# Optimization experiments

Hardware: AMD Instinct MI355X
Metric: run time of the kernel (lower is better)

Reference implementation:

```python
import jax, jax.numpy as jnp
import numpy as np

B, S, D = 2, 2048, 1024
H = 16
DK = D // H
SCALE = 1.0 / np.sqrt(DK)

def setup_inputs() -> dict:
    key = jax.random.key(0)
    ks = jax.random.split(key, 11)
    std = 1.0 / np.sqrt(D)
    return {
        "query": jax.random.normal(ks[0], (B, S, D), jnp.float32),
        "key":   jax.random.normal(ks[1], (B, S, D), jnp.float32),
        "value": jax.random.normal(ks[2], (B, S, D), jnp.float32),
        "Wq": jax.random.normal(ks[3], (D, H * DK), jnp.float32) * std,
        "bq": jnp.zeros((H * DK,), jnp.float32),
        "Wk": jax.random.normal(ks[4], (D, H * DK), jnp.float32) * std,
        "bk": jnp.zeros((H * DK,), jnp.float32),
        "Wv": jax.random.normal(ks[5], (D, H * DK), jnp.float32) * std,
        "bv": jnp.zeros((H * DK,), jnp.float32),
        "Wo": jax.random.normal(ks[6], (D, D), jnp.float32) * std,
        "bo": jnp.zeros((D,), jnp.float32),
    }

def reference(query, key, value, Wq, bq, Wk, bk, Wv, bv, Wo, bo):
    b, s, _ = query.shape
    # projections -> [b, s, h, d_k]
    q = (query @ Wq + bq).reshape(b, s, H, DK)
    k = (key   @ Wk + bk).reshape(b, s, H, DK)
    v = (value @ Wv + bv).reshape(b, s, H, DK)
    # scores [b, i, j, h]
    scores = jnp.einsum('bihd,bjhd->bijh', q, k) * SCALE
    attn = jax.nn.softmax(scores, axis=2)  # softmax over key dim j
    # dropout rate 0.0 (eval mode) -> identity
    x = jnp.einsum('bijh,bjhd->bihd', attn, v).reshape(b, s, H * DK)
    return x @ Wo + bo
```

## Files before the change

kernel.cpp:

```cpp
#include <hip/hip_runtime.h>
#include <hip/hip_bf16.h>
#include <math.h>
#include <stdint.h>

constexpr int Bb = 2, Ss = 2048, Dd = 1024, Hh = 16;
constexpr int Mm = Bb * Ss;
constexpr int Nn = Dd;
constexpr int Kk = Dd;
constexpr float QSCALE = 0.125f * 1.44269504088896340736f;

typedef unsigned short ushort_t;
typedef __attribute__((ext_vector_type(8))) short bf16x8;
typedef __attribute__((ext_vector_type(4))) float f32x4;

#if __has_builtin(__builtin_amdgcn_exp2f)
#define EXP2F(x) __builtin_amdgcn_exp2f(x)
#else
#define EXP2F(x) exp2f(x)
#endif

__device__ __forceinline__ ushort_t f2bf(float f) {
  union { float f; unsigned u; } v; v.f = f;
  return (ushort_t)((v.u + 0x7fff + ((v.u >> 16) & 1)) >> 16);
}

__device__ __forceinline__ void load16_lds(const void* g, void* l) {
  __builtin_amdgcn_global_load_lds(
      (const __attribute__((address_space(1))) void*)(uintptr_t)g,
      (__attribute__((address_space(3))) void*)(uint32_t)(uintptr_t)l, 16, 0, 0);
}

__global__ __launch_bounds__(256) void prep(
    const float* __restrict__ q, const float* __restrict__ k,
    const float* __restrict__ v, ushort_t* __restrict__ qkvb,
    const float* __restrict__ Wq, const float* __restrict__ Wk,
    const float* __restrict__ Wv, const float* __restrict__ Wo,
    ushort_t* __restrict__ Wt) {
  const int bid = blockIdx.x;
  const int tid = threadIdx.x;
  if (bid < 12288) {
    const int z = bid >> 12, xi = bid & 4095;
    const float* src = (z == 0) ? q : (z == 1) ? k : v;
    ushort_t* dst = qkvb + (size_t)z * Mm * Kk;
    const size_t idx = ((size_t)xi * 256 + tid) * 4;
    const float4 val = *(const float4*)(src + idx);
    ushort4 o;
    o.x = f2bf(val.x); o.y = f2bf(val.y); o.z = f2bf(val.z); o.w = f2bf(val.w);
    *(ushort4*)(dst + idx) = o;
    return;
  }
  const int bid2 = bid - 12288;
  const int z = bid2 >> 8, rem = bid2 & 255;
  const float* W = (z == 0) ? Wq : (z == 1) ? Wk : (z == 2) ? Wv : Wo;
  ushort_t* out = Wt + (size_t)z * Kk * Nn;
  __shared__ float t[64][65];
  const int n0 = (rem & 15) * 64, k0 = (rem >> 4) * 64;
  const int lr = tid >> 4, lc = (tid & 15) * 4;
#pragma unroll
  for (int i = 0; i < 4; i++) {
    const int r = lr + i * 16;
    const float4 vv = *(const float4*)(W + (size_t)(k0 + r) * Nn + n0 + lc);
    t[r][lc] = vv.x; t[r][lc + 1] = vv.y; t[r][lc + 2] = vv.z; t[r][lc + 3] = vv.w;
  }
  __syncthreads();
  const int n = tid >> 2, kc = (tid & 3) * 16;
  ushort_t tmp[16];
#pragma unroll
  for (int j = 0; j < 16; j++) tmp[j] = f2bf(t[kc + j][n]);
  ushort_t* op = out + (size_t)(n0 + n) * Kk + k0 + kc;
  ((uint4*)op)[0] = ((uint4*)tmp)[0];
  ((uint4*)op)[1] = ((uint4*)tmp)[1];
}

__global__ __launch_bounds__(256) void transpose_v(
    const ushort_t* __restrict__ Vp, ushort_t* __restrict__ Vt) {
  __shared__ ushort_t t[64][68];
  const int tid = threadIdx.x;
  const int s0 = blockIdx.x * 64, h = blockIdx.y, b = blockIdx.z;
  const int lr = tid >> 4, lc = (tid & 15) * 4;
#pragma unroll
  for (int i = 0; i < 4; i++) {
    const int r = lr + i * 16;
    const ushort4 v =
        *(const ushort4*)(Vp + (size_t)(b * Ss + s0 + r) * Dd + h * 64 + lc);
    *(ushort4*)&t[r][lc] = v;
  }
  __syncthreads();
  const int d = tid >> 2, sc = (tid & 3) * 16;
  ushort_t tmp[16];
#pragma unroll
  for (int j = 0; j < 16; j++) tmp[j] = t[sc + j][d];
  ushort_t* op = Vt + ((size_t)b * Dd + h * 64 + d) * Ss + s0 + sc;
  ((uint4*)op)[0] = ((uint4*)tmp)[0];
  ((uint4*)op)[1] = ((uint4*)tmp)[1];
}

template <int BN, bool OUT_BF16>
__global__ __launch_bounds__(256) void gemm_mfma(
    const ushort_t* __restrict__ Abase, size_t a_stride,
    const ushort_t* __restrict__ Wbase, size_t w_stride,
    const float* __restrict__ bias0, const float* __restrict__ bias1,
    const float* __restrict__ bias2, void* __restrict__ Cbase, size_t c_stride,
    float scale_z0) {
  constexpr int BM = 128, BK = 32;
  constexpr int WM = (BN == 128) ? 64 : 32;
  constexpr int MT_ = WM / 16, NT_ = 4;
  __shared__ ushort_t As[BM * BK];
  __shared__ ushort_t Bs[BN * BK];
  const int tid = threadIdx.x, lane = tid & 63, wid = tid >> 6;
  const int z = blockIdx.z;
  const ushort_t* A = Abase + (size_t)z * a_stride;
  const ushort_t* Wt = Wbase + (size_t)z * w_stride;
  const float* bias = (z == 0) ? bias0 : (z == 1) ? bias1 : bias2;
  const float sc = (z == 0) ? scale_z0 : 1.0f;
  const int m0 = blockIdx.y * BM, n0 = blockIdx.x * BN;
  const int wm = (BN == 128) ? (wid >> 1) * 64 : wid * 32;
  const int wn = (BN == 128) ? (wid & 1) * 64 : 0;
  const int quad = lane >> 4, r16 = lane & 15;
  const int srow = lane >> 2;
  const int scol = (lane & 3) * 8;

  f32x4 acc[MT_][NT_];
#pragma unroll
  for (int m = 0; m < MT_; m++)
#pragma unroll
    for (int n = 0; n < NT_; n++) acc[m][n] = f32x4{0.f, 0.f, 0.f, 0.f};

  for (int k0 = 0; k0 < Kk; k0 += BK) {
    __syncthreads();
#pragma unroll
    for (int i = 0; i < BM / 64; i++) {
      const int I = wid * (BM / 64) + i;
      load16_lds(A + (size_t)(m0 + I * 16 + srow) * Kk + k0 + scol, As + I * 512);
    }
#pragma unroll
    for (int i = 0; i < BN / 64; i++) {
      const int I = wid * (BN / 64) + i;
      load16_lds(Wt + (size_t)(n0 + I * 16 + srow) * Kk + k0 + scol, Bs + I * 512);
    }
    __syncthreads();
    bf16x8 af[MT_], bfr[NT_];
#pragma unroll
    for (int m = 0; m < MT_; m++)
      af[m] = *(const bf16x8*)(As + (wm + m * 16 + r16) * BK + quad * 8);
#pragma unroll
    for (int n = 0; n < NT_; n++)
      bfr[n] = *(const bf16x8*)(Bs + (wn + n * 16 + r16) * BK + quad * 8);
#pragma unroll
    for (int m = 0; m < MT_; m++)
#pragma unroll
      for (int n = 0; n < NT_; n++)
        acc[m][n] =
            __builtin_amdgcn_mfma_f32_16x16x32_bf16(af[m], bfr[n], acc[m][n], 0, 0, 0);
  }

#pragma unroll
  for (int m = 0; m < MT_; m++) {
#pragma unroll
    for (int n = 0; n < NT_; n++) {
      const int gc = n0 + wn + n * 16 + r16;
      const float bv = bias[gc];
#pragma unroll
      for (int r = 0; r < 4; r++) {
        const int gr = m0 + wm + m * 16 + quad * 4 + r;
        const float v = (acc[m][n][r] + bv) * sc;
        if (OUT_BF16)
          ((ushort_t*)Cbase)[(size_t)z * c_stride + (size_t)gr * Nn + gc] = f2bf(v);
        else
          ((float*)Cbase)[(size_t)z * c_stride + (size_t)gr * Nn + gc] = v;
      }
    }
  }
}

__global__ __launch_bounds__(256) void flash_mfma(
    const ushort_t* __restrict__ Qp, const ushort_t* __restrict__ Kp,
    const ushort_t* __restrict__ Vt, ushort_t* __restrict__ Xp) {
  __shared__ ushort_t Ks[64 * 64];
  __shared__ ushort_t Vts[64 * 64];
  __shared__ ushort_t Ps[64 * 72];
  const int tid = threadIdx.x, lane = tid & 63, wid = tid >> 6;
  const int qt = blockIdx.x, h = blockIdx.y, b = blockIdx.z;
  const int quad = lane >> 4, r16 = lane & 15;
  const int row8 = lane >> 3;
  const int colsw = ((lane & 7) ^ (row8 & 7)) * 8;
  const int swz = r16 & 7;

  const int qrow = wid * 16 + r16;
  const ushort_t* Qg = Qp + ((size_t)(b * Ss + qt * 64)) * Dd + h * 64;
  const ushort_t* Kg = Kp + ((size_t)b * Ss) * Dd + h * 64;
  const ushort_t* Vg = Vt + ((size_t)b * Dd + h * 64) * Ss;

  bf16x8 qf[2];
#pragma unroll
  for (int ks = 0; ks < 2; ks++)
    qf[ks] = *(const bf16x8*)(Qg + (size_t)qrow * Dd + ks * 32 + quad * 8);

  f32x4 acc[4];
  float rs = 0.f;
#pragma unroll
  for (int mt = 0; mt < 4; mt++) acc[mt] = f32x4{0.f, 0.f, 0.f, 0.f};

  for (int kt = 0; kt < Ss / 64; kt++) {
    __syncthreads();
#pragma unroll
    for (int i = 0; i < 2; i++) {
      const int I = wid * 2 + i;
      load16_lds(Kg + (size_t)(kt * 64 + I * 8 + row8) * Dd + colsw, Ks + I * 512);
      load16_lds(Vg + (size_t)(I * 8 + row8) * Ss + kt * 64 + colsw, Vts + I * 512);
    }
    __syncthreads();

    f32x4 sacc[4];
#pragma unroll
    for (int mm = 0; mm < 4; mm++) sacc[mm] = f32x4{0.f, 0.f, 0.f, 0.f};
#pragma unroll
    for (int ks = 0; ks < 2; ks++) {
      const int ko = ((ks * 4 + quad) ^ swz) * 8;
      bf16x8 kf[4];
#pragma unroll
      for (int mm = 0; mm < 4; mm++)
        kf[mm] = *(const bf16x8*)(Ks + (mm * 16 + r16) * 64 + ko);
#pragma unroll
      for (int mm = 0; mm < 4; mm++)
        sacc[mm] = __builtin_amdgcn_mfma_f32_16x16x32_bf16(
            kf[mm], qf[ks], sacc[mm], 0, 0, 0);
    }

#pragma unroll
    for (int mm = 0; mm < 4; mm++) {
      float p0 = EXP2F(sacc[mm][0]), p1 = EXP2F(sacc[mm][1]);
      float p2 = EXP2F(sacc[mm][2]), p3 = EXP2F(sacc[mm][3]);
      rs += (p0 + p1) + (p2 + p3);
      union { __hip_bfloat162 hh; unsigned u; } lo, hi;
      lo.hh = __float22bfloat162_rn(make_float2(p0, p1));
      hi.hh = __float22bfloat162_rn(make_float2(p2, p3));
      *(uint2*)(Ps + qrow * 72 + mm * 16 + quad * 4) = make_uint2(lo.u, hi.u);
    }

#pragma unroll
    for (int ks = 0; ks < 2; ks++) {
      const int ko = ((ks * 4 + quad) ^ swz) * 8;
      bf16x8 vf[4];
#pragma unroll
      for (int mt = 0; mt < 4; mt++)
        vf[mt] = *(const bf16x8*)(Vts + (mt * 16 + r16) * 64 + ko);
      const bf16x8 pf = *(const bf16x8*)(Ps + qrow * 72 + ks * 32 + quad * 8);
#pragma unroll
      for (int mt = 0; mt < 4; mt++)
        acc[mt] = __builtin_amdgcn_mfma_f32_16x16x32_bf16(
            vf[mt], pf, acc[mt], 0, 0, 0);
    }
  }

  rs += __shfl_xor(rs, 16, 64);
  rs += __shfl_xor(rs, 32, 64);
  const float inv = 1.0f / rs;

#pragma unroll
  for (int mt = 0; mt < 4; mt++) {
    ushort4 o;
    o.x = f2bf(acc[mt][0] * inv);
    o.y = f2bf(acc[mt][1] * inv);
    o.z = f2bf(acc[mt][2] * inv);
    o.w = f2bf(acc[mt][3] * inv);
    *(ushort4*)(Xp + (size_t)(b * Ss + qt * 64 + qrow) * Dd +
                h * 64 + mt * 16 + quad * 4) = o;
  }
}

extern "C" void kernel_launch(void* const* d_in, const int* in_sizes, int n_in,
                              void* d_out, int out_size, void* d_ws,
                              size_t ws_size, hipStream_t stream) {
  const float* q  = (const float*)d_in[0];
  const float* k  = (const float*)d_in[1];
  const float* v  = (const float*)d_in[2];
  const float* Wq = (const float*)d_in[3];
  const float* bq = (const float*)d_in[4];
  const float* Wk = (const float*)d_in[5];
  const float* bk = (const float*)d_in[6];
  const float* Wv = (const float*)d_in[7];
  const float* bv = (const float*)d_in[8];
  const float* Wo = (const float*)d_in[9];
  const float* bo = (const float*)d_in[10];

  ushort_t* ws = (ushort_t*)d_ws;
  const size_t MD = (size_t)Mm * Kk;
  const size_t KN = (size_t)Kk * Nn;
  ushort_t* qkvb = ws;
  ushort_t* Wt   = ws + 3 * MD;
  ushort_t* QKVp = Wt + 4 * KN;
  ushort_t* Vtp  = QKVp + 3 * MD;
  ushort_t* Xp   = qkvb;

  prep<<<dim3(13312), 256, 0, stream>>>(q, k, v, qkvb, Wq, Wk, Wv, Wo, Wt);
  gemm_mfma<128, true><<<dim3(Nn / 128, Mm / 128, 3), 256, 0, stream>>>(
      qkvb, MD, Wt, KN, bq, bk, bv, QKVp, MD, QSCALE);
  transpose_v<<<dim3(Ss / 64, Hh, Bb), 256, 0, stream>>>(QKVp + 2 * MD, Vtp);
  flash_mfma<<<dim3(Ss / 64, Hh, Bb), 256, 0, stream>>>(QKVp, QKVp + MD, Vtp, Xp);
  gemm_mfma<64, false><<<dim3(Nn / 64, Mm / 128, 1), 256, 0, stream>>>(
      Xp, 0, Wt + 3 * KN, 0, bo, bo, bo, d_out, 0, 1.0f);
}
```

Baseline: 237.3 us.

## Double-buffer K/V tiles in flash attention with async prefetch and block swizzle

Changes the flash attention loop to double-buffer K and V tiles in LDS, issuing the next tile's global-to-LDS loads before computing the current one and waiting with explicit vmcnt plus a barrier. Also remaps block indices so neighbouring workgroups share heads for cache locality, XOR-swizzles the P scratch buffer instead of padding it to cut bank conflicts, and raises wave priority around the MFMA sections. The aim is to hide global load latency behind compute. In exchange LDS use roughly doubles, which may reduce occupancy, and correctness now depends on hand-written waitcnt counts.

```diff
diff --git a/kernel.cpp b/kernel.cpp
--- a/kernel.cpp
+++ b/kernel.cpp
@@ -176,15 +176,18 @@
 __global__ __launch_bounds__(256) void flash_mfma(
     const ushort_t* __restrict__ Qp, const ushort_t* __restrict__ Kp,
     const ushort_t* __restrict__ Vt, ushort_t* __restrict__ Xp) {
-  __shared__ ushort_t Ks[64 * 64];
-  __shared__ ushort_t Vts[64 * 64];
-  __shared__ ushort_t Ps[64 * 72];
+  __shared__ ushort_t Ks[2][64 * 64];
+  __shared__ ushort_t Vts[2][64 * 64];
+  __shared__ ushort_t Ps[64 * 64];
   const int tid = threadIdx.x, lane = tid & 63, wid = tid >> 6;
-  const int qt = blockIdx.x, h = blockIdx.y, b = blockIdx.z;
+  const int lid = blockIdx.x + (blockIdx.y << 5) + (blockIdx.z << 9);
+  const int swzb = ((lid & 7) << 7) + (lid >> 3);
+  const int qt = swzb & 31, h = (swzb >> 5) & 15, b = swzb >> 9;
   const int quad = lane >> 4, r16 = lane & 15;
   const int row8 = lane >> 3;
   const int colsw = ((lane & 7) ^ (row8 & 7)) * 8;
   const int swz = r16 & 7;
+  const int psw2 = (r16 & 7) * 2;
 
   const int qrow = wid * 16 + r16;
   const ushort_t* Qg = Qp + ((size_t)(b * Ss + qt * 64)) * Dd + h * 64;
@@ -201,31 +204,46 @@
 #pragma unroll
   for (int mt = 0; mt < 4; mt++) acc[mt] = f32x4{0.f, 0.f, 0.f, 0.f};
 
-  for (int kt = 0; kt < Ss / 64; kt++) {
-    __syncthreads();
+  auto stage = [&](int kt, int bsel) {
 #pragma unroll
     for (int i = 0; i < 2; i++) {
       const int I = wid * 2 + i;
-      load16_lds(Kg + (size_t)(kt * 64 + I * 8 + row8) * Dd + colsw, Ks + I * 512);
-      load16_lds(Vg + (size_t)(I * 8 + row8) * Ss + kt * 64 + colsw, Vts + I * 512);
-    }
-    __syncthreads();
+      load16_lds(Kg + (size_t)(kt * 64 + I * 8 + row8) * Dd + colsw,
+                 &Ks[bsel][I * 512]);
+      load16_lds(Vg + (size_t)(I * 8 + row8) * Ss + kt * 64 + colsw,
+                 &Vts[bsel][I * 512]);
+    }
+  };
+
+  stage(0, 0);
+  asm volatile("s_waitcnt vmcnt(4)" ::: "memory");
+
+  for (int kt = 0; kt < Ss / 64; kt++) {
+    const int cur = kt & 1;
+    if (kt + 1 < Ss / 64) {
+      stage(kt + 1, cur ^ 1);
+      asm volatile("s_waitcnt vmcnt(4)\n\ts_barrier" ::: "memory");
+    } else {
+      asm volatile("s_waitcnt vmcnt(0)\n\ts_barrier" ::: "memory");
+    }
 
     f32x4 sacc[4];
 #pragma unroll
     for (int mm = 0; mm < 4; mm++) sacc[mm] = f32x4{0.f, 0.f, 0.f, 0.f};
+    __builtin_amdgcn_s_setprio(1);
 #pragma unroll
     for (int ks = 0; ks < 2; ks++) {
       const int ko = ((ks * 4 + quad) ^ swz) * 8;
       bf16x8 kf[4];
 #pragma unroll
       for (int mm = 0; mm < 4; mm++)
-        kf[mm] = *(const bf16x8*)(Ks + (mm * 16 + r16) * 64 + ko);
+        kf[mm] = *(const bf16x8*)(&Ks[cur][(mm * 16 + r16) * 64 + ko]);
 #pragma unroll
       for (int mm = 0; mm < 4; mm++)
         sacc[mm] = __builtin_amdgcn_mfma_f32_16x16x32_bf16(
             kf[mm], qf[ks], sacc[mm], 0, 0, 0);
     }
+    __builtin_amdgcn_s_setprio(0);
 
 #pragma unroll
     for (int mm = 0; mm < 4; mm++) {
@@ -235,22 +253,28 @@
       union { __hip_bfloat162 hh; unsigned u; } lo, hi;
       lo.hh = __float22bfloat162_rn(make_float2(p0, p1));
       hi.hh = __float22bfloat162_rn(make_float2(p2, p3));
-      *(uint2*)(Ps + qrow * 72 + mm * 16 + quad * 4) = make_uint2(lo.u, hi.u);
-    }
-
+      *(uint2*)(Ps + qrow * 64 + (((mm * 4 + quad) ^ psw2) << 2)) =
+          make_uint2(lo.u, hi.u);
+    }
+
+    __builtin_amdgcn_s_setprio(1);
 #pragma unroll
     for (int ks = 0; ks < 2; ks++) {
       const int ko = ((ks * 4 + quad) ^ swz) * 8;
       bf16x8 vf[4];
 #pragma unroll
       for (int mt = 0; mt < 4; mt++)
-        vf[mt] = *(const bf16x8*)(Vts + (mt * 16 + r16) * 64 + ko);
-      const bf16x8 pf = *(const bf16x8*)(Ps + qrow * 72 + ks * 32 + quad * 8);
+        vf[mt] = *(const bf16x8*)(&Vts[cur][(mt * 16 + r16) * 64 + ko]);
+      const bf16x8 pf = *(const bf16x8*)(
+          Ps + qrow * 64 + ((((ks * 4 + quad) << 1) ^ psw2) << 2));
 #pragma unroll
       for (int mt = 0; mt < 4; mt++)
         acc[mt] = __builtin_amdgcn_mfma_f32_16x16x32_bf16(
             vf[mt], pf, acc[mt], 0, 0, 0);
     }
+    __builtin_amdgcn_s_setprio(0);
+
+    asm volatile("s_barrier" ::: "memory");
   }
 
   rs += __shfl_xor(rs, 16, 64);
```

After: 239.1 us. About the same (+0.8%).
